# Performance work log

Hardware: AMD Instinct MI355X
Metric: run time of the kernel (lower is better)

The kernel has to match this reference:

```python
import jax, jax.numpy as jnp
import numpy as np

B, T, H, DK, DV = 4, 2048, 1024, 1024, 1024


def setup_inputs() -> dict:
    key = jax.random.key(0)
    ks = jax.random.split(key, 9)
    s = lambda fan_in: 1.0 / np.sqrt(fan_in)
    return {
        "y_all": jax.random.normal(ks[0], (B, T, H), dtype=jnp.float32),
        "Wq": jax.random.uniform(ks[1], (H, DK), jnp.float32, -s(H), s(H)),
        "bq": jax.random.uniform(ks[2], (DK,), jnp.float32, -s(H), s(H)),
        "Wk": jax.random.uniform(ks[3], (H, DK), jnp.float32, -s(H), s(H)),
        "bk": jax.random.uniform(ks[4], (DK,), jnp.float32, -s(H), s(H)),
        "Wv": jax.random.uniform(ks[5], (H, DV), jnp.float32, -s(H), s(H)),
        "bv": jax.random.uniform(ks[6], (DV,), jnp.float32, -s(H), s(H)),
        "Wo": jax.random.uniform(ks[7], (DV, H), jnp.float32, -s(DV), s(DV)),
        "bo": jax.random.uniform(ks[8], (H,), jnp.float32, -s(DV), s(DV)),
    }


def reference(y_all, Wq, bq, Wk, bk, Wv, bv, Wo, bo):
    # Fused causal attention equivalent to the per-timestep Python loop.
    dk = Wq.shape[1]
    q = (y_all @ Wq + bq) / jnp.sqrt(jnp.asarray(dk, y_all.dtype))  # [B,T,DK]
    k = y_all @ Wk + bk                                             # [B,T,DK]
    v = y_all @ Wv + bv                                             # [B,T,DV]
    scores = jnp.einsum("bqd,bkd->bqk", q, k)                       # [B,T,T]
    t = y_all.shape[1]
    causal = jnp.tril(jnp.ones((t, t), dtype=bool))                 # [T,T]
    scores = jnp.where(causal[None], scores, jnp.asarray(-jnp.inf, scores.dtype))
    w = jax.nn.softmax(scores, axis=-1)                             # [B,T,T]
    ctx = jnp.einsum("bqk,bkd->bqd", w, v)                          # [B,T,DV]
    return ctx @ Wo + bo                                            # [B,T,H]
```

## Files before the change

kernel.cpp:

```cpp
#include <hip/hip_runtime.h>
#include <hip/hip_bf16.h>
#include <cstdint>

#define DEVI __device__ __forceinline__

typedef __attribute__((ext_vector_type(8))) short bf16x8;
typedef __attribute__((ext_vector_type(4))) short bf16x4;
typedef __attribute__((ext_vector_type(4))) float f32x4;

template<int I> struct IC { static constexpr int v = I; };

DEVI short f2bf(float f) {
  unsigned u = __float_as_uint(f);
  u += 0x7fff + ((u >> 16) & 1);
  return (short)(u >> 16);
}
DEVI float bf2f(short s) { return __uint_as_float(((unsigned)(unsigned short)s) << 16); }

DEVI void gl_lds16(const short* g, short* l) {
  __builtin_amdgcn_global_load_lds((const __attribute__((address_space(1))) unsigned*)g,
                                   (__attribute__((address_space(3))) unsigned*)l, 16, 0, 0);
}

DEVI void bar() {
  asm volatile("" ::: "memory");
  __builtin_amdgcn_s_barrier();
  asm volatile("" ::: "memory");
}

__global__ __launch_bounds__(512, 1)
void gemm_qkproj_8ph(const short* __restrict__ A, const short* __restrict__ B,
                     short* __restrict__ C, const float* __restrict__ b0,
                     const float* __restrict__ b1, float scale,
                     int K, int lda, int ldb, int ldc, int tilesN)
{
  const int nwg = gridDim.x, orig = blockIdx.x;
  const int q8 = nwg >> 3, r8 = nwg & 7;
  const int xcd = orig & 7, idx8 = orig >> 3;
  const int wg = (xcd < r8 ? xcd * (q8 + 1) : r8 * (q8 + 1) + (xcd - r8) * q8) + idx8;
  const int bi = wg / tilesN, bj = wg - bi * tilesN;

  __shared__ __align__(16) short lA[4][8192];
  __shared__ __align__(16) short lB[4][8192];

  const int tid = threadIdx.x, wave = tid >> 6, lane = tid & 63;
  const int wm = wave >> 2, wn = wave & 3;
  const int fr = lane & 15, h = lane >> 4;
  const int brow = bi * 256, bcol = bj * 256;

  const int ck = (h ^ ((fr >> 1) & 3)) * 8;
  const int aBase = (wm * 128 + fr) * 32 + ck;
  const int bBase = (wn * 64 + fr) * 32 + ck;

  const int swc = ((tid & 3) ^ ((tid >> 3) & 3)) * 8;
  const short* pa = A + (long long)(brow + (tid >> 2)) * lda + swc;
  const short* pb = B + (long long)(bcol + (tid >> 2)) * ldb + swc;

  f32x4 acc[8][4] = {};
  const int nt = K / 64;

  auto stgA = [&](auto SL, int koff) {
    constexpr int s = decltype(SL)::v;
    gl_lds16(pa + koff,                  &lA[s][tid * 8]);
    gl_lds16(pa + koff + 128 * (long long)lda, &lA[s][4096 + tid * 8]);
  };
  auto stgB = [&](auto SL, int koff) {
    constexpr int s = decltype(SL)::v;
    gl_lds16(pb + koff,                  &lB[s][tid * 8]);
    gl_lds16(pb + koff + 128 * (long long)ldb, &lB[s][4096 + tid * 8]);
  };

  stgA(IC<0>{}, 0);   stgB(IC<0>{}, 0);
  stgA(IC<1>{}, 32);  stgB(IC<1>{}, 32);
  stgA(IC<2>{}, 64);  stgB(IC<2>{}, 64);
  stgA(IC<3>{}, 96);
  asm volatile("s_waitcnt vmcnt(6)" ::: "memory");
  bar();

  auto group = [&](auto PC, int t) {
    constexpr int P  = decltype(PC)::v;
    constexpr int s0 = 2 * P, s1 = 2 * P + 1;
    constexpr int ob1 = 2 * (P ^ 1) + 1;
    const bool st1 = (t + 1 < nt), st2 = (t + 2 < nt);
    const int k2 = (t + 2) * 64;
    bf16x8 a[4], a2[4], b[4];

#pragma unroll
    for (int m = 0; m < 4; ++m) a[m]  = *(const bf16x8*)&lA[s0][aBase + (m * 16) * 32];
#pragma unroll
    for (int m = 0; m < 4; ++m) a2[m] = *(const bf16x8*)&lA[s0][aBase + (64 + m * 16) * 32];
#pragma unroll
    for (int n = 0; n < 4; ++n) b[n]  = *(const bf16x8*)&lB[s0][bBase + (n * 16) * 32];
    if (st1) stgB(IC<ob1>{}, (t + 1) * 64 + 32);
    if (st2) stgA(IC<s0>{}, k2);
    bar();
    asm volatile("s_waitcnt lgkmcnt(0)" ::: "memory");
    __builtin_amdgcn_sched_barrier(0);
    __builtin_amdgcn_s_setprio(1);
#pragma unroll
    for (int m = 0; m < 4; ++m)
#pragma unroll
      for (int n = 0; n < 4; ++n)
        acc[m][n] = __builtin_amdgcn_mfma_f32_16x16x32_bf16(a[m], b[n], acc[m][n], 0, 0, 0);
#pragma unroll
    for (int m = 0; m < 4; ++m)
#pragma unroll
      for (int n = 0; n < 4; ++n)
        acc[m + 4][n] = __builtin_amdgcn_mfma_f32_16x16x32_bf16(a2[m], b[n], acc[m + 4][n], 0, 0, 0);
    __builtin_amdgcn_s_setprio(0);
    bar();

#pragma unroll
    for (int m = 0; m < 4; ++m) a[m]  = *(const bf16x8*)&lA[s1][aBase + (m * 16) * 32];
#pragma unroll
    for (int m = 0; m < 4; ++m) a2[m] = *(const bf16x8*)&lA[s1][aBase + (64 + m * 16) * 32];
#pragma unroll
    for (int n = 0; n < 4; ++n) b[n]  = *(const bf16x8*)&lB[s1][bBase + (n * 16) * 32];
    if (st2) { stgB(IC<s0>{}, k2); stgA(IC<s1>{}, k2 + 32); }
    bar();
    asm volatile("s_waitcnt lgkmcnt(0)" ::: "memory");
    __builtin_amdgcn_sched_barrier(0);
    __builtin_amdgcn_s_setprio(1);
#pragma unroll
    for (int m = 0; m < 4; ++m)
#pragma unroll
      for (int n = 0; n < 4; ++n)
        acc[m][n] = __builtin_amdgcn_mfma_f32_16x16x32_bf16(a[m], b[n], acc[m][n], 0, 0, 0);
#pragma unroll
    for (int m = 0; m < 4; ++m)
#pragma unroll
      for (int n = 0; n < 4; ++n)
        acc[m + 4][n] = __builtin_amdgcn_mfma_f32_16x16x32_bf16(a2[m], b[n], acc[m + 4][n], 0, 0, 0);
    __builtin_amdgcn_s_setprio(0);
    if (st2)      asm volatile("s_waitcnt vmcnt(6)" ::: "memory");
    else if (st1) asm volatile("s_waitcnt vmcnt(0)" ::: "memory");
    if (st1) bar();
  };

  for (int t = 0; t + 1 < nt; t += 2) { group(IC<0>{}, t); group(IC<1>{}, t + 1); }

  int   colg[4]; float bvv[4], scl[4];
#pragma unroll
  for (int n = 0; n < 4; ++n) {
    colg[n] = bcol + wn * 64 + n * 16 + fr;
    const int seg = colg[n] >> 10;
    bvv[n] = seg ? b1[colg[n] & 1023] : b0[colg[n] & 1023];
    scl[n] = seg ? 1.f : scale;
  }
#pragma unroll
  for (int m = 0; m < 8; ++m) {
    const int row = brow + wm * 128 + m * 16 + h * 4;
#pragma unroll
    for (int j = 0; j < 4; ++j) {
      short* cr = C + (long long)(row + j) * ldc;
#pragma unroll
      for (int n = 0; n < 4; ++n)
        cr[colg[n]] = f2bf((acc[m][n][j] + bvv[n]) * scl[n]);
    }
  }
}

constexpr int BM = 128, BN = 128, BK = 64;

template<int MODE, int BIASMODE, bool OUTF32, int DECODE>
__global__ __launch_bounds__(256, 2)
void gemm_bt(const short* __restrict__ A, const short* __restrict__ B,
             void* __restrict__ Cv, const float* __restrict__ b0,
             float scale, int K, int lda, int ldb, int ldc,
             long long sA, long long sB, long long sC, int tdim)
{
  const int nwg = gridDim.x, orig = blockIdx.x;
  const int q8 = nwg >> 3, r8 = nwg & 7;
  const int xcd = orig & 7, idx8 = orig >> 3;
  const int wg = (xcd < r8 ? xcd * (q8 + 1) : r8 * (q8 + 1) + (xcd - r8) * q8) + idx8;
  const int bz = blockIdx.z;

  int bi, bj;
  if constexpr (MODE == 4) {
    int b = (int)((__fsqrt_rn(8.f * (float)wg + 1.f) - 1.f) * 0.5f);
    if ((b + 1) * (b + 2) / 2 <= wg) ++b;
    if (b * (b + 1) / 2 > wg) --b;
    bi = b; bj = wg - b * (b + 1) / 2;
  } else {
    bi = wg / tdim;
    bj = wg - bi * tdim;
    if constexpr (DECODE == 2) bi = (nwg / tdim) - 1 - bi;
    if constexpr (DECODE == 3) { if (bz & 2) bi = (nwg / tdim) - 1 - bi; }
  }

  A += (long long)bz * sA;
  B += (long long)bz * sB;

  __shared__ __align__(16) short lA[2][BM * BK];
  __shared__ __align__(16) short lB[2][BN * BK];

  const int tid = threadIdx.x, wave = tid >> 6, lane = tid & 63;
  const int wr = wave >> 1, wc = wave & 1;
  const int brow = bi * BM, bcol = bj * BN;
  const int fr = lane & 15, h = lane >> 4;

  const int ck0 = ((h ^ (fr & 7))) * 8;
  const int swc = ((tid & 7) ^ ((tid >> 3) & 7)) * 8;
  const short* pA = A + (long long)(brow + (tid >> 3)) * lda + swc;
  const short* pB = B + (long long)(bcol + (tid >> 3)) * ldb + swc;

  f32x4 acc[4][4] = {};
  const int kend = (MODE == 2) ? (bi + 1) * BM : K;
  const int nt = kend / BK;

  auto stage = [&](int buf, int t) {
    const long long ko = (long long)t * BK;
#pragma unroll
    for (int j = 0; j < 4; ++j)
      gl_lds16(pA + (long long)(j * 32) * lda + ko, &lA[buf][j * 2048 + tid * 8]);
#pragma unroll
    for (int j = 0; j < 4; ++j)
      gl_lds16(pB + (long long)(j * 32) * ldb + ko, &lB[buf][j * 2048 + tid * 8]);
  };

  stage(0, 0);
  __syncthreads();

  int cur = 0;
  for (int t = 0; t < nt; ++t) {
    if (t + 1 < nt) stage(cur ^ 1, t + 1);

    const short* bufA = lA[cur];
    const short* bufB = lB[cur];
    bf16x8 af[4], bg[4];
#pragma unroll
    for (int m = 0; m < 4; ++m)
      af[m] = *(const bf16x8*)&bufA[(wr * 64 + m * 16 + fr) * BK + ck0];
#pragma unroll
    for (int n = 0; n < 4; ++n)
      bg[n] = *(const bf16x8*)&bufB[(wc * 64 + n * 16 + fr) * BK + ck0];
#pragma unroll
    for (int m = 0; m < 4; ++m)
#pragma unroll
      for (int n = 0; n < 4; ++n)
        acc[m][n] = __builtin_amdgcn_mfma_f32_16x16x32_bf16(af[m], bg[n], acc[m][n], 0, 0, 0);
#pragma unroll
    for (int m = 0; m < 4; ++m)
      af[m] = *(const bf16x8*)&bufA[((wr * 64 + m * 16 + fr) * BK + ck0) ^ 32];
#pragma unroll
    for (int n = 0; n < 4; ++n)
      bg[n] = *(const bf16x8*)&bufB[((wc * 64 + n * 16 + fr) * BK + ck0) ^ 32];
#pragma unroll
    for (int m = 0; m < 4; ++m)
#pragma unroll
      for (int n = 0; n < 4; ++n)
        acc[m][n] = __builtin_amdgcn_mfma_f32_16x16x32_bf16(af[m], bg[n], acc[m][n], 0, 0, 0);

    __syncthreads();
    cur ^= 1;
  }

  const int lrow = h * 4;
  float* Cf = (float*)Cv + (long long)bz * sC;
  short* Cs = (short*)Cv + (long long)bz * sC;
  int colg[4]; float bvv[4];
#pragma unroll
  for (int n = 0; n < 4; ++n) {
    colg[n] = bcol + wc * 64 + n * 16 + fr;
    bvv[n] = (BIASMODE == 1) ? b0[colg[n]] : 0.f;
  }
#pragma unroll
  for (int m = 0; m < 4; ++m) {
    const int row = brow + wr * 64 + m * 16 + lrow;
#pragma unroll
    for (int j = 0; j < 4; ++j) {
#pragma unroll
      for (int n = 0; n < 4; ++n) {
        const float val = (acc[m][n][j] + bvv[n]) * scale;
        if constexpr (OUTF32) Cf[(long long)(row + j) * ldc + colg[n]] = val;
        else                  Cs[(long long)(row + j) * ldc + colg[n]] = f2bf(val);
      }
    }
  }
}

__global__ __launch_bounds__(256)
void softmax_causal_bf16_k(short* __restrict__ sc)
{
  const int T = 2048;
  const long long row = blockIdx.x;
  const int t = (int)(row & (T - 1));
  short* ps = sc + row * (long long)T;
  const int tid = threadIdx.x, wave = tid >> 6, lane = tid & 63;
  const int c0 = tid * 8;
  const int wlim = ((t >> 7) + 1) << 7;

  bf16x8 v = {};
  if (c0 <= t) v = *(const bf16x8*)&ps[c0];
  float x[8];
#pragma unroll
  for (int j = 0; j < 8; ++j) x[j] = bf2f(v[j]);

  float mx = -3.0e38f;
#pragma unroll
  for (int j = 0; j < 8; ++j) if (c0 + j <= t) mx = fmaxf(mx, x[j]);
#pragma unroll
  for (int o = 32; o; o >>= 1) mx = fmaxf(mx, __shfl_xor(mx, o, 64));
  __shared__ float red[8];
  if (lane == 0) red[wave] = mx;
  __syncthreads();
  const float M = fmaxf(fmaxf(red[0], red[1]), fmaxf(red[2], red[3]));

  float e[8], s = 0.f;
#pragma unroll
  for (int j = 0; j < 8; ++j) { e[j] = (c0 + j <= t) ? __expf(x[j] - M) : 0.f; s += e[j]; }
#pragma unroll
  for (int o = 32; o; o >>= 1) s += __shfl_xor(s, o, 64);
  if (lane == 0) red[4 + wave] = s;
  __syncthreads();
  const float inv = 1.f / (red[4] + red[5] + red[6] + red[7]);

  if (c0 < wlim) {
    bf16x8 ov;
#pragma unroll
    for (int j = 0; j < 8; ++j) ov[j] = f2bf(e[j] * inv);
    *(bf16x8*)&ps[c0] = ov;
  }
}

__global__ __launch_bounds__(256)
void cvt_yT_k(const float* __restrict__ y, short* __restrict__ ybf,
              short* __restrict__ yTb)
{
  __shared__ float tile[32][33];
  const int tx = threadIdx.x & 31, ty = threadIdx.x >> 5;
  const int h0 = blockIdx.x * 32, t0 = blockIdx.y * 32;
  const float* ip = y + (long long)blockIdx.z * 2048 * 1024;
  short* op  = ybf + (long long)blockIdx.z * 2048 * 1024;
  short* opT = yTb + (long long)blockIdx.z * 1024 * 2048;
#pragma unroll
  for (int i = 0; i < 4; ++i) {
    const float f = ip[(long long)(t0 + ty + 8 * i) * 1024 + h0 + tx];
    tile[ty + 8 * i][tx] = f;
    op[(long long)(t0 + ty + 8 * i) * 1024 + h0 + tx] = f2bf(f);
  }
  __syncthreads();
#pragma unroll
  for (int i = 0; i < 4; ++i)
    opT[(long long)(h0 + ty + 8 * i) * 2048 + t0 + tx] = f2bf(tile[tx][ty + 8 * i]);
}

__global__ __launch_bounds__(256)
void cvt_w_all_k(const float* __restrict__ w0, const float* __restrict__ w1,
                 const float* __restrict__ w2, const float* __restrict__ w3,
                 short* __restrict__ o0, short* __restrict__ o1,
                 short* __restrict__ o2, short* __restrict__ o3)
{
  const int tx = threadIdx.x & 31, ty = threadIdx.x >> 5;
  const int r0 = blockIdx.y * 32, c0 = blockIdx.x * 32;
  if (blockIdx.z == 3) {
#pragma unroll
    for (int i = 0; i < 4; ++i)
      o3[(long long)(r0 + ty + 8 * i) * 1024 + c0 + tx] =
          f2bf(w3[(long long)(r0 + ty + 8 * i) * 1024 + c0 + tx]);
    return;
  }
  const float* in = (blockIdx.z == 0) ? w0 : (blockIdx.z == 1 ? w1 : w2);
  short* out      = (blockIdx.z == 0) ? o0 : (blockIdx.z == 1 ? o1 : o2);
  __shared__ float tile[32][33];
#pragma unroll
  for (int i = 0; i < 4; ++i)
    tile[ty + 8 * i][tx] = in[(long long)(r0 + ty + 8 * i) * 1024 + c0 + tx];
  __syncthreads();
#pragma unroll
  for (int i = 0; i < 4; ++i)
    out[(long long)(c0 + ty + 8 * i) * 1024 + r0 + tx] = f2bf(tile[tx][ty + 8 * i]);
}

__global__ __launch_bounds__(256)
void bias_init_k(const float* __restrict__ bo, float* __restrict__ outb)
{
  const int j = blockIdx.x * 256 + threadIdx.x;
  outb[j] = bo[j];
}

__global__ __launch_bounds__(256)
void bias_fold_k(const float* __restrict__ bv, const float* __restrict__ Wo,
                 float* __restrict__ outb)
{
  const int r0 = blockIdx.x * 16;
  const int c4 = threadIdx.x;
  float4 acc = make_float4(0.f, 0.f, 0.f, 0.f);
  for (int r = 0; r < 16; ++r) {
    const float s = bv[r0 + r];
    const float4 w = ((const float4*)(Wo + (long long)(r0 + r) * 1024))[c4];
    acc.x += s * w.x; acc.y += s * w.y; acc.z += s * w.z; acc.w += s * w.w;
  }
  atomicAdd(&outb[c4 * 4 + 0], acc.x);
  atomicAdd(&outb[c4 * 4 + 1], acc.y);
  atomicAdd(&outb[c4 * 4 + 2], acc.z);
  atomicAdd(&outb[c4 * 4 + 3], acc.w);
}

__global__ __launch_bounds__(256)
void combine4_k(const float* __restrict__ p, short* __restrict__ out)
{
  const long long i = (long long)blockIdx.x * 256 + threadIdx.x;
  const float4 a = ((const float4*)p)[i];
  const float4 b = ((const float4*)(p + 1048576))[i];
  const float4 c = ((const float4*)(p + 2097152))[i];
  const float4 d = ((const float4*)(p + 3145728))[i];
  bf16x4 o;
  o[0] = f2bf(a.x + b.x + c.x + d.x);
  o[1] = f2bf(a.y + b.y + c.y + d.y);
  o[2] = f2bf(a.z + b.z + c.z + d.z);
  o[3] = f2bf(a.w + b.w + c.w + d.w);
  ((bf16x4*)out)[i] = o;
}

extern "C" void kernel_launch(void* const* d_in, const int* in_sizes, int n_in,
                              void* d_out, int out_size, void* d_ws, size_t ws_size,
                              hipStream_t stream)
{
  (void)in_sizes; (void)n_in; (void)out_size; (void)ws_size;
  const float* y  = (const float*)d_in[0];
  const float* Wq = (const float*)d_in[1];
  const float* bq = (const float*)d_in[2];
  const float* Wk = (const float*)d_in[3];
  const float* bk = (const float*)d_in[4];
  const float* Wv = (const float*)d_in[5];
  const float* bv = (const float*)d_in[6];
  const float* Wo = (const float*)d_in[7];
  const float* bo = (const float*)d_in[8];
  float* out = (float*)d_out;

  const int T = 2048, H = 1024, DK = 1024;
  const long long MT = 8192;

  short* ws    = (short*)d_ws;
  short* ybf   = ws;
  short* WqkT  = ybf + MT * H;
  short* WoT   = WqkT + 2ll * 1024 * 1024;
  short* WvBf  = WoT + 1024ll * 1024;
  short* WvoT  = WvBf + 1024ll * 1024;
  short* QKb   = WvoT + 1024ll * 1024;
  short* yTb   = QKb + MT * 2048;
  short* scores = yTb + MT * 1024;
  float* bvWoBo = (float*)(scores + 4ll * T * T);
  float* wvoPart = bvWoBo + 1024;
  short* ctxY  = ybf;

  cvt_yT_k<<<dim3(32, 64, 4), 256, 0, stream>>>(y, ybf, yTb);
  cvt_w_all_k<<<dim3(32, 32, 4), 256, 0, stream>>>(
      Wq, Wk, Wo, Wv, WqkT, WqkT + 1024ll * 1024, WoT, WvBf);
  bias_init_k<<<4, 256, 0, stream>>>(bo, bvWoBo);
  bias_fold_k<<<64, 256, 0, stream>>>(bv, Wo, bvWoBo);

  gemm_bt<0, 0, true, 0><<<dim3(64, 1, 4), 256, 0, stream>>>(
      WoT, WvBf, wvoPart, nullptr, 1.f, 256, 1024, 1024, 1024,
      256, 256, 1048576, 8);
  combine4_k<<<1024, 256, 0, stream>>>(wvoPart, WvoT);

  gemm_qkproj_8ph<<<dim3(32 * 8, 1, 1), 512, 0, stream>>>(
      ybf, WqkT, QKb, bq, bk, 1.f / 32.f, H, H, H, 2048, 8);

  gemm_bt<4, 0, false, 0><<<dim3(136, 1, 4), 256, 0, stream>>>(
      QKb, QKb + 1024, scores, nullptr, 1.f, DK, 2048, 2048, T,
      (long long)T * 2048, (long long)T * 2048, (long long)T * T, 16);

  softmax_causal_bf16_k<<<(int)MT, 256, 0, stream>>>(scores);

  gemm_bt<2, 0, false, 3><<<dim3(16 * 8, 1, 4), 256, 0, stream>>>(
      scores, yTb, ctxY, nullptr, 1.f, T, T, 2048, 1024,
      (long long)T * T, 1024ll * 2048, (long long)T * 1024, 8);

  gemm_bt<0, 1, true, 0><<<dim3(64 * 8, 1, 1), 256, 0, stream>>>(
      ctxY, WvoT, out, bvWoBo, 1.f, 1024, 1024, 1024, 1024, 0, 0, 0, 8);
}
```

Baseline: 190.9 us.

## Reassociate output projection before attention and drop custom QK projection kernel

The final projection is moved ahead of attention. y is first multiplied by the folded Wv·Wo to form zT, and the P·V GEMM then writes the fp32 output directly with the folded bias. This removes the transposed copy of y and the separate ctx@Wvo GEMM. The QK projection now reuses the generic 128x128 gemm_bt kernel with a new per-column bias/scale mode instead of the specialised 256x256 8-phase kernel, and the y conversion becomes a plain vectorised cast. The cost is an extra 8192x1024x1024 GEMM producing zT, and possibly a slower QK projection than the tuned kernel.

```diff
diff --git a/kernel.cpp b/kernel.cpp
--- a/kernel.cpp
+++ b/kernel.cpp
@@ -7,8 +7,6 @@
 typedef __attribute__((ext_vector_type(8))) short bf16x8;
 typedef __attribute__((ext_vector_type(4))) short bf16x4;
 typedef __attribute__((ext_vector_type(4))) float f32x4;
-
-template<int I> struct IC { static constexpr int v = I; };
 
 DEVI short f2bf(float f) {
   unsigned u = __float_as_uint(f);
@@ -22,151 +20,14 @@
                                    (__attribute__((address_space(3))) unsigned*)l, 16, 0, 0);
 }
 
-DEVI void bar() {
-  asm volatile("" ::: "memory");
-  __builtin_amdgcn_s_barrier();
-  asm volatile("" ::: "memory");
-}
-
-__global__ __launch_bounds__(512, 1)
-void gemm_qkproj_8ph(const short* __restrict__ A, const short* __restrict__ B,
-                     short* __restrict__ C, const float* __restrict__ b0,
-                     const float* __restrict__ b1, float scale,
-                     int K, int lda, int ldb, int ldc, int tilesN)
-{
-  const int nwg = gridDim.x, orig = blockIdx.x;
-  const int q8 = nwg >> 3, r8 = nwg & 7;
-  const int xcd = orig & 7, idx8 = orig >> 3;
-  const int wg = (xcd < r8 ? xcd * (q8 + 1) : r8 * (q8 + 1) + (xcd - r8) * q8) + idx8;
-  const int bi = wg / tilesN, bj = wg - bi * tilesN;
-
-  __shared__ __align__(16) short lA[4][8192];
-  __shared__ __align__(16) short lB[4][8192];
-
-  const int tid = threadIdx.x, wave = tid >> 6, lane = tid & 63;
-  const int wm = wave >> 2, wn = wave & 3;
-  const int fr = lane & 15, h = lane >> 4;
-  const int brow = bi * 256, bcol = bj * 256;
-
-  const int ck = (h ^ ((fr >> 1) & 3)) * 8;
-  const int aBase = (wm * 128 + fr) * 32 + ck;
-  const int bBase = (wn * 64 + fr) * 32 + ck;
-
-  const int swc = ((tid & 3) ^ ((tid >> 3) & 3)) * 8;
-  const short* pa = A + (long long)(brow + (tid >> 2)) * lda + swc;
-  const short* pb = B + (long long)(bcol + (tid >> 2)) * ldb + swc;
-
-  f32x4 acc[8][4] = {};
-  const int nt = K / 64;
-
-  auto stgA = [&](auto SL, int koff) {
-    constexpr int s = decltype(SL)::v;
-    gl_lds16(pa + koff,                  &lA[s][tid * 8]);
-    gl_lds16(pa + koff + 128 * (long long)lda, &lA[s][4096 + tid * 8]);
-  };
-  auto stgB = [&](auto SL, int koff) {
-    constexpr int s = decltype(SL)::v;
-    gl_lds16(pb + koff,                  &lB[s][tid * 8]);
-    gl_lds16(pb + koff + 128 * (long long)ldb, &lB[s][4096 + tid * 8]);
-  };
-
-  stgA(IC<0>{}, 0);   stgB(IC<0>{}, 0);
-  stgA(IC<1>{}, 32);  stgB(IC<1>{}, 32);
-  stgA(IC<2>{}, 64);  stgB(IC<2>{}, 64);
-  stgA(IC<3>{}, 96);
-  asm volatile("s_waitcnt vmcnt(6)" ::: "memory");
-  bar();
-
-  auto group = [&](auto PC, int t) {
-    constexpr int P  = decltype(PC)::v;
-    constexpr int s0 = 2 * P, s1 = 2 * P + 1;
-    constexpr int ob1 = 2 * (P ^ 1) + 1;
-    const bool st1 = (t + 1 < nt), st2 = (t + 2 < nt);
-    const int k2 = (t + 2) * 64;
-    bf16x8 a[4], a2[4], b[4];
-
-#pragma unroll
-    for (int m = 0; m < 4; ++m) a[m]  = *(const bf16x8*)&lA[s0][aBase + (m * 16) * 32];
-#pragma unroll
-    for (int m = 0; m < 4; ++m) a2[m] = *(const bf16x8*)&lA[s0][aBase + (64 + m * 16) * 32];
-#pragma unroll
-    for (int n = 0; n < 4; ++n) b[n]  = *(const bf16x8*)&lB[s0][bBase + (n * 16) * 32];
-    if (st1) stgB(IC<ob1>{}, (t + 1) * 64 + 32);
-    if (st2) stgA(IC<s0>{}, k2);
-    bar();
-    asm volatile("s_waitcnt lgkmcnt(0)" ::: "memory");
-    __builtin_amdgcn_sched_barrier(0);
-    __builtin_amdgcn_s_setprio(1);
-#pragma unroll
-    for (int m = 0; m < 4; ++m)
-#pragma unroll
-      for (int n = 0; n < 4; ++n)
-        acc[m][n] = __builtin_amdgcn_mfma_f32_16x16x32_bf16(a[m], b[n], acc[m][n], 0, 0, 0);
-#pragma unroll
-    for (int m = 0; m < 4; ++m)
-#pragma unroll
-      for (int n = 0; n < 4; ++n)
-        acc[m + 4][n] = __builtin_amdgcn_mfma_f32_16x16x32_bf16(a2[m], b[n], acc[m + 4][n], 0, 0, 0);
-    __builtin_amdgcn_s_setprio(0);
-    bar();
-
-#pragma unroll
-    for (int m = 0; m < 4; ++m) a[m]  = *(const bf16x8*)&lA[s1][aBase + (m * 16) * 32];
-#pragma unroll
-    for (int m = 0; m < 4; ++m) a2[m] = *(const bf16x8*)&lA[s1][aBase + (64 + m * 16) * 32];
-#pragma unroll
-    for (int n = 0; n < 4; ++n) b[n]  = *(const bf16x8*)&lB[s1][bBase + (n * 16) * 32];
-    if (st2) { stgB(IC<s0>{}, k2); stgA(IC<s1>{}, k2 + 32); }
-    bar();
-    asm volatile("s_waitcnt lgkmcnt(0)" ::: "memory");
-    __builtin_amdgcn_sched_barrier(0);
-    __builtin_amdgcn_s_setprio(1);
-#pragma unroll
-    for (int m = 0; m < 4; ++m)
-#pragma unroll
-      for (int n = 0; n < 4; ++n)
-        acc[m][n] = __builtin_amdgcn_mfma_f32_16x16x32_bf16(a[m], b[n], acc[m][n], 0, 0, 0);
-#pragma unroll
-    for (int m = 0; m < 4; ++m)
-#pragma unroll
-      for (int n = 0; n < 4; ++n)
-        acc[m + 4][n] = __builtin_amdgcn_mfma_f32_16x16x32_bf16(a2[m], b[n], acc[m + 4][n], 0, 0, 0);
-    __builtin_amdgcn_s_setprio(0);
-    if (st2)      asm volatile("s_waitcnt vmcnt(6)" ::: "memory");
-    else if (st1) asm volatile("s_waitcnt vmcnt(0)" ::: "memory");
-    if (st1) bar();
-  };
-
-  for (int t = 0; t + 1 < nt; t += 2) { group(IC<0>{}, t); group(IC<1>{}, t + 1); }
-
-  int   colg[4]; float bvv[4], scl[4];
-#pragma unroll
-  for (int n = 0; n < 4; ++n) {
-    colg[n] = bcol + wn * 64 + n * 16 + fr;
-    const int seg = colg[n] >> 10;
-    bvv[n] = seg ? b1[colg[n] & 1023] : b0[colg[n] & 1023];
-    scl[n] = seg ? 1.f : scale;
-  }
-#pragma unroll
-  for (int m = 0; m < 8; ++m) {
-    const int row = brow + wm * 128 + m * 16 + h * 4;
-#pragma unroll
-    for (int j = 0; j < 4; ++j) {
-      short* cr = C + (long long)(row + j) * ldc;
-#pragma unroll
-      for (int n = 0; n < 4; ++n)
-        cr[colg[n]] = f2bf((acc[m][n][j] + bvv[n]) * scl[n]);
-    }
-  }
-}
-
 constexpr int BM = 128, BN = 128, BK = 64;
 
 template<int MODE, int BIASMODE, bool OUTF32, int DECODE>
 __global__ __launch_bounds__(256, 2)
 void gemm_bt(const short* __restrict__ A, const short* __restrict__ B,
              void* __restrict__ Cv, const float* __restrict__ b0,
-             float scale, int K, int lda, int ldb, int ldc,
+             const float* __restrict__ b1, float scale,
+             int K, int lda, int ldb, int ldc,
              long long sA, long long sB, long long sC, int tdim)
 {
   const int nwg = gridDim.x, orig = blockIdx.x;
@@ -184,7 +45,6 @@
   } else {
     bi = wg / tdim;
     bj = wg - bi * tdim;
-    if constexpr (DECODE == 2) bi = (nwg / tdim) - 1 - bi;
     if constexpr (DECODE == 3) { if (bz & 2) bi = (nwg / tdim) - 1 - bi; }
   }
 
@@ -258,11 +118,16 @@
   const int lrow = h * 4;
   float* Cf = (float*)Cv + (long long)bz * sC;
   short* Cs = (short*)Cv + (long long)bz * sC;
-  int colg[4]; float bvv[4];
+  int colg[4]; float bvv[4], scl[4];
 #pragma unroll
   for (int n = 0; n < 4; ++n) {
     colg[n] = bcol + wc * 64 + n * 16 + fr;
-    bvv[n] = (BIASMODE == 1) ? b0[colg[n]] : 0.f;
+    if constexpr (BIASMODE == 1) { bvv[n] = b0[colg[n]]; scl[n] = scale; }
+    else if constexpr (BIASMODE == 2) {
+      const int seg = colg[n] >> 10;
+      bvv[n] = seg ? b1[colg[n] & 1023] : b0[colg[n] & 1023];
+      scl[n] = seg ? 1.f : scale;
+    } else { bvv[n] = 0.f; scl[n] = scale; }
   }
 #pragma unroll
   for (int m = 0; m < 4; ++m) {
@@ -271,7 +136,7 @@
     for (int j = 0; j < 4; ++j) {
 #pragma unroll
       for (int n = 0; n < 4; ++n) {
-        const float val = (acc[m][n][j] + bvv[n]) * scale;
+        const float val = (acc[m][n][j] + bvv[n]) * scl[n];
         if constexpr (OUTF32) Cf[(long long)(row + j) * ldc + colg[n]] = val;
         else                  Cs[(long long)(row + j) * ldc + colg[n]] = f2bf(val);
       }
@@ -324,25 +189,15 @@
 }
 
 __global__ __launch_bounds__(256)
-void cvt_yT_k(const float* __restrict__ y, short* __restrict__ ybf,
-              short* __restrict__ yTb)
-{
-  __shared__ float tile[32][33];
-  const int tx = threadIdx.x & 31, ty = threadIdx.x >> 5;
-  const int h0 = blockIdx.x * 32, t0 = blockIdx.y * 32;
-  const float* ip = y + (long long)blockIdx.z * 2048 * 1024;
-  short* op  = ybf + (long long)blockIdx.z * 2048 * 1024;
-  short* opT = yTb + (long long)blockIdx.z * 1024 * 2048;
-#pragma unroll
-  for (int i = 0; i < 4; ++i) {
-    const float f = ip[(long long)(t0 + ty + 8 * i) * 1024 + h0 + tx];
-    tile[ty + 8 * i][tx] = f;
-    op[(long long)(t0 + ty + 8 * i) * 1024 + h0 + tx] = f2bf(f);
-  }
-  __syncthreads();
-#pragma unroll
-  for (int i = 0; i < 4; ++i)
-    opT[(long long)(h0 + ty + 8 * i) * 2048 + t0 + tx] = f2bf(tile[tx][ty + 8 * i]);
+void cvt_y_k(const float* __restrict__ y, short* __restrict__ ybf)
+{
+  const long long i = (long long)blockIdx.x * 256 + threadIdx.x;
+  const float4 v0 = ((const float4*)y)[i * 2];
+  const float4 v1 = ((const float4*)y)[i * 2 + 1];
+  bf16x8 o;
+  o[0] = f2bf(v0.x); o[1] = f2bf(v0.y); o[2] = f2bf(v0.z); o[3] = f2bf(v0.w);
+  o[4] = f2bf(v1.x); o[5] = f2bf(v1.y); o[6] = f2bf(v1.z); o[7] = f2bf(v1.w);
+  ((bf16x8*)ybf)[i] = o;
 }
 
 __global__ __launch_bounds__(256)
@@ -439,36 +294,36 @@
   short* WvBf  = WoT + 1024ll * 1024;
   short* WvoT  = WvBf + 1024ll * 1024;
   short* QKb   = WvoT + 1024ll * 1024;
-  short* yTb   = QKb + MT * 2048;
-  short* scores = yTb + MT * 1024;
+  short* zT    = QKb + MT * 2048;
+  short* scores = zT + MT * 1024;
   float* bvWoBo = (float*)(scores + 4ll * T * T);
   float* wvoPart = bvWoBo + 1024;
-  short* ctxY  = ybf;
-
-  cvt_yT_k<<<dim3(32, 64, 4), 256, 0, stream>>>(y, ybf, yTb);
+
+  cvt_y_k<<<4096, 256, 0, stream>>>(y, ybf);
   cvt_w_all_k<<<dim3(32, 32, 4), 256, 0, stream>>>(
       Wq, Wk, Wo, Wv, WqkT, WqkT + 1024ll * 1024, WoT, WvBf);
   bias_init_k<<<4, 256, 0, stream>>>(bo, bvWoBo);
   bias_fold_k<<<64, 256, 0, stream>>>(bv, Wo, bvWoBo);
 
   gemm_bt<0, 0, true, 0><<<dim3(64, 1, 4), 256, 0, stream>>>(
-      WoT, WvBf, wvoPart, nullptr, 1.f, 256, 1024, 1024, 1024,
+      WoT, WvBf, wvoPart, nullptr, nullptr, 1.f, 256, 1024, 1024, 1024,
       256, 256, 1048576, 8);
   combine4_k<<<1024, 256, 0, stream>>>(wvoPart, WvoT);
 
-  gemm_qkproj_8ph<<<dim3(32 * 8, 1, 1), 512, 0, stream>>>(
-      ybf, WqkT, QKb, bq, bk, 1.f / 32.f, H, H, H, 2048, 8);
+  gemm_bt<0, 2, false, 0><<<dim3(64 * 16, 1, 1), 256, 0, stream>>>(
+      ybf, WqkT, QKb, bq, bk, 1.f / 32.f, H, H, H, 2048, 0, 0, 0, 16);
+
+  gemm_bt<0, 0, false, 0><<<dim3(512, 1, 1), 256, 0, stream>>>(
+      WvoT, ybf, zT, nullptr, nullptr, 1.f, 1024, 1024, 1024, 8192,
+      0, 0, 0, 64);
 
   gemm_bt<4, 0, false, 0><<<dim3(136, 1, 4), 256, 0, stream>>>(
-      QKb, QKb + 1024, scores, nullptr, 1.f, DK, 2048, 2048, T,
+      QKb, QKb + 1024, scores, nullptr, nullptr, 1.f, DK, 2048, 2048, T,
       (long long)T * 2048, (long long)T * 2048, (long long)T * T, 16);
 
   softmax_causal_bf16_k<<<(int)MT, 256, 0, stream>>>(scores);
 
-  gemm_bt<2, 0, false, 3><<<dim3(16 * 8, 1, 4), 256, 0, stream>>>(
-      scores, yTb, ctxY, nullptr, 1.f, T, T, 2048, 1024,
-      (long long)T * T, 1024ll * 2048, (long long)T * 1024, 8);
-
-  gemm_bt<0, 1, true, 0><<<dim3(64 * 8, 1, 1), 256, 0, stream>>>(
-      ctxY, WvoT, out, bvWoBo, 1.f, 1024, 1024, 1024, 1024, 0, 0, 0, 8);
-}
+  gemm_bt<2, 1, true, 3><<<dim3(16 * 8, 1, 4), 256, 0, stream>>>(
+      scores, zT, out, bvWoBo, nullptr, 1.f, T, T, 8192, 1024,
+      (long long)T * T, 2048, 2048ll * 1024, 8);
+}
```

New measurement: 193.0 us. No clear change (+1.1%).
